# Optimization experiments

Measured on AMD Instinct MI355X. Metric: run time of the kernel, lower is better.

Reference implementation:

```python
import jax, jax.numpy as jnp
import numpy as np

N, E, F, H = 131072, 524288, 128, 128
EPS = 1e-5

def _gcn(x, W, b, src, dst, ew):
    # GCNConv with normalize=False: linear -> gather -> edge-weight scale -> scatter-add -> bias
    h = x @ W                                  # [N, H]
    msg = h[src] * ew[:, None]                 # [E, H]
    return jax.ops.segment_sum(msg, dst, num_segments=N) + b

def _ln(x, g, b):
    mu = jnp.mean(x, axis=-1, keepdims=True)
    var = jnp.var(x, axis=-1, keepdims=True)
    return (x - mu) * jax.lax.rsqrt(var + EPS) * g + b

def setup_inputs() -> dict:
    key = jax.random.key(0)
    ks = jax.random.split(key, 32)
    d = {}
    d['x'] = jax.random.normal(ks[0], (N, F), dtype=jnp.float32)
    names = ['fwd', 'ons', 'sus', 'rest']
    for i, t in enumerate(names):
        d['ei_' + t] = jax.random.randint(ks[1 + i], (2, E), 0, N)
        d['ew_' + t] = jax.random.uniform(ks[5 + i], (E,), dtype=jnp.float32)
        d['W1_' + t] = jax.random.normal(ks[9 + i], (F, H), dtype=jnp.float32) * 0.1
        d['b1_' + t] = jnp.zeros((H,), dtype=jnp.float32)
        d['W2_' + t] = jax.random.normal(ks[13 + i], (H, H), dtype=jnp.float32) * 0.1
        d['b2_' + t] = jnp.zeros((H,), dtype=jnp.float32)
    d['g1'] = jnp.ones((H,), dtype=jnp.float32)
    d['be1'] = jnp.zeros((H,), dtype=jnp.float32)
    d['g2'] = jnp.ones((H,), dtype=jnp.float32)
    d['be2'] = jnp.zeros((H,), dtype=jnp.float32)
    return d

def reference(x, ei_fwd, ei_ons, ei_sus, ei_rest,
              ew_fwd, ew_ons, ew_sus, ew_rest,
              W1_fwd, b1_fwd, W2_fwd, b2_fwd,
              W1_ons, b1_ons, W2_ons, b2_ons,
              W1_sus, b1_sus, W2_sus, b2_sus,
              W1_rest, b1_rest, W2_rest, b2_rest,
              g1, be1, g2, be2):
    eis = [ei_fwd, ei_ons, ei_sus, ei_rest]
    ews = [ew_fwd, ew_ons, ew_sus, ew_rest]
    W1s = [W1_fwd, W1_ons, W1_sus, W1_rest]
    b1s = [b1_fwd, b1_ons, b1_sus, b1_rest]
    W2s = [W2_fwd, W2_ons, W2_sus, W2_rest]
    b2s = [b2_fwd, b2_ons, b2_sus, b2_rest]
    # HeteroConv aggr='sum' over the 4 edge types
    h = sum(_gcn(x, W1s[i], b1s[i], eis[i][0], eis[i][1], ews[i]) for i in range(4))
    h = _ln(h, g1, be1)  # dropout is identity in eval/reference mode
    h2 = sum(_gcn(h, W2s[i], b2s[i], eis[i][0], eis[i][1], ews[i]) for i in range(4))
    return _ln(h2, g2, be2)
```

## Files before the change

kernel.cpp:

```cpp
#include <hip/hip_runtime.h>
#include <hip/hip_fp16.h>

#define NN 131072
#define EE 524288

typedef _Float16 f16x8 __attribute__((ext_vector_type(8)));
typedef float f32x4 __attribute__((ext_vector_type(4)));

__device__ __forceinline__ unsigned short f2h(float f) {
  __half h = __float2half(f);
  unsigned short r;
  __builtin_memcpy(&r, &h, 2);
  return r;
}
__device__ __forceinline__ __half2 u2h2(unsigned u) {
  __half2 h;
  __builtin_memcpy(&h, &u, 4);
  return h;
}
__device__ __forceinline__ unsigned h22u(__half2 h) {
  unsigned u;
  __builtin_memcpy(&u, &h, 4);
  return u;
}

__global__ __launch_bounds__(256) void khc(const int* __restrict__ d0, const int* __restrict__ d1,
                                           const int* __restrict__ d2, const int* __restrict__ d3,
                                           unsigned* __restrict__ gc) {
  __shared__ unsigned h[512];
  for (int i = threadIdx.x; i < 512; i += 256) h[i] = 0;
  __syncthreads();
  unsigned base = blockIdx.x * 2048u + threadIdx.x;
#pragma unroll
  for (int k = 0; k < 8; ++k) {
    unsigned e = base + k * 256u;
    unsigned t = e >> 19, i = e & (EE - 1u);
    const int* dd = (t == 0) ? d0 : (t == 1) ? d1 : (t == 2) ? d2 : d3;
    atomicAdd(&h[((unsigned)dd[i]) >> 8], 1u);
  }
  __syncthreads();
  for (int i = threadIdx.x; i < 512; i += 256) atomicAdd(&gc[i], h[i]);
}

__global__ __launch_bounds__(512) void kscan_small(const unsigned* __restrict__ gc, unsigned* __restrict__ rpc,
                                                   unsigned* __restrict__ cursor, unsigned* __restrict__ rp_fine) {
  __shared__ unsigned sh[512];
  int tid = threadIdx.x;
  unsigned x = gc[tid];
  sh[tid] = x;
  __syncthreads();
  for (int o = 1; o < 512; o <<= 1) {
    unsigned v = (tid >= o) ? sh[tid - o] : 0u;
    __syncthreads();
    sh[tid] += v;
    __syncthreads();
  }
  unsigned excl = sh[tid] - x;
  rpc[tid] = excl;
  cursor[tid] = excl;
  if (tid == 511) rpc[512] = sh[511];
  if (tid == 0) rp_fine[4u * NN] = 4u * EE;
}

__global__ __launch_bounds__(256) void kbinA(
    const int* __restrict__ e0, const int* __restrict__ e1, const int* __restrict__ e2, const int* __restrict__ e3,
    const float* __restrict__ w0, const float* __restrict__ w1, const float* __restrict__ w2, const float* __restrict__ w3,
    unsigned* __restrict__ cursor, uint2* __restrict__ tmp) {
  __shared__ unsigned hist[512];
  __shared__ unsigned base[512];
  int tid = threadIdx.x;
  unsigned t = blockIdx.x >> 7;
  unsigned chunk = blockIdx.x & 127u;
  const int* ei = (t == 0) ? e0 : (t == 1) ? e1 : (t == 2) ? e2 : e3;
  const float* ew = (t == 0) ? w0 : (t == 1) ? w1 : (t == 2) ? w2 : w3;
  const int* srcp = ei;
  const int* dstp = ei + EE;
  unsigned ib = chunk * 4096u;
  for (int i = tid; i < 512; i += 256) hist[i] = 0;
  __syncthreads();
  unsigned km[16], sm[16];
  float wm[16];
#pragma unroll
  for (int k = 0; k < 16; ++k) {
    unsigned i = ib + k * 256u + tid;
    unsigned dst = (unsigned)dstp[i];
    sm[k] = (unsigned)srcp[i];
    wm[k] = ew[i];
    km[k] = (dst << 2) | t;
    atomicAdd(&hist[dst >> 8], 1u);
  }
  __syncthreads();
  for (int j = tid; j < 512; j += 256) {
    unsigned c = hist[j];
    base[j] = c ? atomicAdd(&cursor[j], c) : 0u;
    hist[j] = 0u;
  }
  __syncthreads();
#pragma unroll
  for (int k = 0; k < 16; ++k) {
    unsigned b = km[k] >> 10;
    unsigned l = atomicAdd(&hist[b], 1u);
    tmp[(size_t)base[b] + l] = make_uint2(sm[k] | ((km[k] & 1023u) << 17), __float_as_uint(wm[k]));
  }
}

__global__ __launch_bounds__(256) void kbinB(const unsigned* __restrict__ rpc, const uint2* __restrict__ tmp,
                                             unsigned* __restrict__ rp_fine, uint2* __restrict__ edges) {
  __shared__ unsigned cnts[1024];
  __shared__ unsigned ps[256];
  int tid = threadIdx.x;
  unsigned b = blockIdx.x;
  unsigned s = rpc[b], e = rpc[b + 1];
  unsigned cnt = e - s;
  for (int j = tid; j < 1024; j += 256) cnts[j] = 0;
  __syncthreads();
  for (unsigned i = tid; i < cnt; i += 256) {
    unsigned lk = tmp[s + i].x >> 17;
    atomicAdd(&cnts[lk], 1u);
  }
  __syncthreads();
  unsigned c4[4], lsum = 0;
#pragma unroll
  for (int q = 0; q < 4; ++q) { c4[q] = cnts[tid * 4 + q]; lsum += c4[q]; }
  ps[tid] = lsum;
  __syncthreads();
  for (int o = 1; o < 256; o <<= 1) {
    unsigned v = (tid >= o) ? ps[tid - o] : 0u;
    __syncthreads();
    ps[tid] += v;
    __syncthreads();
  }
  unsigned excl = ps[tid] - lsum;
  __syncthreads();
#pragma unroll
  for (int q = 0; q < 4; ++q) {
    rp_fine[b * 1024u + (unsigned)tid * 4u + q] = s + excl;
    cnts[tid * 4 + q] = excl;
    excl += c4[q];
  }
  __syncthreads();
  for (unsigned i = tid; i < cnt; i += 256) {
    uint2 r = tmp[s + i];
    unsigned lk = r.x >> 17;
    unsigned p = atomicAdd(&cnts[lk], 1u);
    edges[(size_t)s + p] = make_uint2(r.x & 0x1ffffu, r.y);
  }
}

__global__ __launch_bounds__(256) void kcast(const float4* __restrict__ x, ushort4* __restrict__ o) {
  unsigned i = blockIdx.x * 256u + threadIdx.x;
  float4 v = x[i];
  ushort4 r;
  r.x = f2h(v.x); r.y = f2h(v.y); r.z = f2h(v.z); r.w = f2h(v.w);
  o[i] = r;
}

__global__ __launch_bounds__(256) void kwconv2(
    const float* __restrict__ m0, const float* __restrict__ m1, const float* __restrict__ m2, const float* __restrict__ m3,
    const float* __restrict__ m4, const float* __restrict__ m5, const float* __restrict__ m6, const float* __restrict__ m7,
    unsigned short* __restrict__ img) {
  unsigned gidx = blockIdx.x * 256u + threadIdx.x;
  unsigned L = gidx >> 16;
  unsigned r = gidx & 65535u;
  unsigned k = r >> 7, c = r & 127u;
  unsigned t = k >> 7, krow = k & 127u;
  const float* W;
  if (L == 0) W = (t == 0) ? m0 : (t == 1) ? m1 : (t == 2) ? m2 : m3;
  else        W = (t == 0) ? m4 : (t == 1) ? m5 : (t == 2) ? m6 : m7;
  img[(size_t)L * 65536 + (k >> 5) * 4096 + c * 32 + ((k & 31u) ^ ((c & 3u) << 3))] = f2h(W[krow * 128 + c]);
}

__global__ __launch_bounds__(128) void kbias(
    const float* __restrict__ a0, const float* __restrict__ a1, const float* __restrict__ a2, const float* __restrict__ a3,
    const float* __restrict__ c0, const float* __restrict__ c1, const float* __restrict__ c2, const float* __restrict__ c3,
    float* __restrict__ bsum) {
  int c = threadIdx.x;
  bsum[c] = a0[c] + a1[c] + a2[c] + a3[c];
  bsum[128 + c] = c0[c] + c1[c] + c2[c] + c3[c];
}

__global__ __launch_bounds__(512) void kfuse(const uint2* __restrict__ edges, const unsigned* __restrict__ rp,
                                             const unsigned short* __restrict__ X,
                                             const unsigned short* __restrict__ Wimg, int layer,
                                             const float* __restrict__ bsum,
                                             const float* __restrict__ gw, const float* __restrict__ bw,
                                             unsigned short* __restrict__ outh, float* __restrict__ outf, int wf32) {
  __shared__ unsigned short sZ[64 * 512];
  __shared__ unsigned short sW[2 * 4096];
  const int tid = threadIdx.x;
  const int wv = tid >> 6;
  const int lane = tid & 63;
  const int g = lane >> 4;
  const int cl = lane & 15;
  const unsigned dbase = blockIdx.x * 64u;

  const unsigned short* Xr = X + (size_t)(cl * 8);
  for (int it = 0; it < 8; ++it) {
    unsigned row = (unsigned)(wv * 8 + it);
    unsigned d = dbase + row;
    unsigned s = rp[d * 4u + g];
    unsigned e = rp[d * 4u + g + 1];
    unsigned len = e - s;
    int m = (int)len;
    m = max(m, __shfl_xor(m, 16, 64));
    m = max(m, __shfl_xor(m, 32, 64));
    __half2 accA[4], accB[4];
    const __half2 z2 = __half2(__half(0.f), __half(0.f));
#pragma unroll
    for (int k = 0; k < 4; ++k) { accA[k] = z2; accB[k] = z2; }
    unsigned jlast = len ? e - 1u : s;
    for (int i = 0; i < m; i += 4) {
      unsigned j[4], sidx[4];
      uint2 q[4];
      __half2 w2[4];
#pragma unroll
      for (int k = 0; k < 4; ++k) {
        bool v = (unsigned)(i + k) < len;
        j[k] = v ? s + (unsigned)(i + k) : jlast;
      }
#pragma unroll
      for (int k = 0; k < 4; ++k) q[k] = edges[j[k]];
#pragma unroll
      for (int k = 0; k < 4; ++k) {
        bool v = (unsigned)(i + k) < len;
        sidx[k] = v ? q[k].x : 0u;
        w2[k] = __float2half2_rn(v ? __uint_as_float(q[k].y) : 0.f);
      }
      uint4 u0 = *(const uint4*)(Xr + (size_t)sidx[0] * 128);
      uint4 u1 = *(const uint4*)(Xr + (size_t)sidx[1] * 128);
      uint4 u2 = *(const uint4*)(Xr + (size_t)sidx[2] * 128);
      uint4 u3 = *(const uint4*)(Xr + (size_t)sidx[3] * 128);
      accA[0] = __hfma2(w2[0], u2h2(u0.x), accA[0]);
      accA[1] = __hfma2(w2[0], u2h2(u0.y), accA[1]);
      accA[2] = __hfma2(w2[0], u2h2(u0.z), accA[2]);
      accA[3] = __hfma2(w2[0], u2h2(u0.w), accA[3]);
      accB[0] = __hfma2(w2[1], u2h2(u1.x), accB[0]);
      accB[1] = __hfma2(w2[1], u2h2(u1.y), accB[1]);
      accB[2] = __hfma2(w2[1], u2h2(u1.z), accB[2]);
      accB[3] = __hfma2(w2[1], u2h2(u1.w), accB[3]);
      accA[0] = __hfma2(w2[2], u2h2(u2.x), accA[0]);
      accA[1] = __hfma2(w2[2], u2h2(u2.y), accA[1]);
      accA[2] = __hfma2(w2[2], u2h2(u2.z), accA[2]);
      accA[3] = __hfma2(w2[2], u2h2(u2.w), accA[3]);
      accB[0] = __hfma2(w2[3], u2h2(u3.x), accB[0]);
      accB[1] = __hfma2(w2[3], u2h2(u3.y), accB[1]);
      accB[2] = __hfma2(w2[3], u2h2(u3.z), accB[2]);
      accB[3] = __hfma2(w2[3], u2h2(u3.w), accB[3]);
    }
    uint4 o;
    o.x = h22u(__hadd2(accA[0], accB[0]));
    o.y = h22u(__hadd2(accA[1], accB[1]));
    o.z = h22u(__hadd2(accA[2], accB[2]));
    o.w = h22u(__hadd2(accA[3], accB[3]));
    *(uint4*)((char*)sZ + row * 1024 + (((unsigned)(g * 256 + cl * 16)) ^ ((row & 7u) << 4))) = o;
  }

  const int rlo = lane & 15;
  const int khi = lane >> 4;
  const int mt = wv >> 1;
  const int nh = wv & 1;
  f32x4 acc[4];
#pragma unroll
  for (int n = 0; n < 4; ++n) acc[n] = (f32x4){0.f, 0.f, 0.f, 0.f};
  const uint4* W2 = (const uint4*)(Wimg + (size_t)layer * 65536);
  const int arow = mt * 16 + rlo;
  for (int st = 0; st < 8; ++st) {
    __syncthreads();
    ((uint4*)sW)[tid * 2] = W2[st * 1024 + tid * 2];
    ((uint4*)sW)[tid * 2 + 1] = W2[st * 1024 + tid * 2 + 1];
    __syncthreads();
#pragma unroll
    for (int kcl = 0; kcl < 2; ++kcl) {
      int kc = st * 2 + kcl;
      f16x8 a = *(const f16x8*)((const char*)sZ + arow * 1024 + (((unsigned)(kc * 64 + khi * 16)) ^ ((arow & 7) << 4)));
#pragma unroll
      for (int n = 0; n < 4; ++n) {
        int cc = nh * 64 + n * 16 + rlo;
        f16x8 b = *(const f16x8*)((const char*)sW + kcl * 8192 + cc * 64 + (((unsigned)(khi * 16)) ^ ((cc & 3) << 4)));
        acc[n] = __builtin_amdgcn_mfma_f32_16x16x32_f16(a, b, acc[n], 0, 0, 0);
      }
    }
  }

  float bs[4], ggv[4], bwv[4];
#pragma unroll
  for (int n = 0; n < 4; ++n) {
    int cc = nh * 64 + n * 16 + rlo;
    bs[n] = bsum[cc];
    ggv[n] = gw[cc];
    bwv[n] = bw[cc];
  }
  float* sPart = (float*)sW;
  __syncthreads();
#pragma unroll
  for (int rg = 0; rg < 4; ++rg) {
    float s1 = 0.f, s2 = 0.f;
#pragma unroll
    for (int n = 0; n < 4; ++n) {
      float v = acc[n][rg] + bs[n];
      s1 += v;
      s2 += v * v;
    }
    s1 += __shfl_xor(s1, 1, 64); s2 += __shfl_xor(s2, 1, 64);
    s1 += __shfl_xor(s1, 2, 64); s2 += __shfl_xor(s2, 2, 64);
    s1 += __shfl_xor(s1, 4, 64); s2 += __shfl_xor(s2, 4, 64);
    s1 += __shfl_xor(s1, 8, 64); s2 += __shfl_xor(s2, 8, 64);
    if (rlo == 0) {
      int row = mt * 16 + khi * 4 + rg;
      sPart[row * 4 + nh * 2] = s1;
      sPart[row * 4 + nh * 2 + 1] = s2;
    }
  }
  __syncthreads();
#pragma unroll
  for (int rg = 0; rg < 4; ++rg) {
    int row = mt * 16 + khi * 4 + rg;
    float s1 = sPart[row * 4 + 0] + sPart[row * 4 + 2];
    float s2 = sPart[row * 4 + 1] + sPart[row * 4 + 3];
    float mu = s1 * (1.f / 128.f);
    float var = fmaxf(s2 * (1.f / 128.f) - mu * mu, 0.f);
    float inv = rsqrtf(var + 1e-5f);
    size_t d = (size_t)dbase + (unsigned)row;
    if (wf32) {
#pragma unroll
      for (int n = 0; n < 4; ++n) {
        int cc = nh * 64 + n * 16 + rlo;
        outf[d * 128 + cc] = (acc[n][rg] + bs[n] - mu) * inv * ggv[n] + bwv[n];
      }
    } else {
#pragma unroll
      for (int n = 0; n < 4; ++n) {
        int cc = nh * 64 + n * 16 + rlo;
        outh[d * 128 + cc] = f2h((acc[n][rg] + bs[n] - mu) * inv * ggv[n] + bwv[n]);
      }
    }
  }
}

extern "C" void kernel_launch(void* const* d_in, const int* in_sizes, int n_in,
                              void* d_out, int out_size, void* d_ws, size_t ws_size,
                              hipStream_t stream) {
  (void)n_in; (void)out_size; (void)ws_size;
  const float* x = (const float*)d_in[0];
  const int* ei[4];
  const float *ew[4], *W1[4], *b1[4], *W2[4], *b2[4];
  const float *g1, *be1, *g2, *be2;
  if (in_sizes[2] == EE) {
    for (int t = 0; t < 4; ++t) {
      int base = 1 + t * 6;
      ei[t] = (const int*)d_in[base + 0];
      ew[t] = (const float*)d_in[base + 1];
      W1[t] = (const float*)d_in[base + 2];
      b1[t] = (const float*)d_in[base + 3];
      W2[t] = (const float*)d_in[base + 4];
      b2[t] = (const float*)d_in[base + 5];
    }
  } else {
    for (int t = 0; t < 4; ++t) {
      ei[t] = (const int*)d_in[1 + t];
      ew[t] = (const float*)d_in[5 + t];
      W1[t] = (const float*)d_in[9 + t * 4 + 0];
      b1[t] = (const float*)d_in[9 + t * 4 + 1];
      W2[t] = (const float*)d_in[9 + t * 4 + 2];
      b2[t] = (const float*)d_in[9 + t * 4 + 3];
    }
  }
  g1 = (const float*)d_in[25];
  be1 = (const float*)d_in[26];
  g2 = (const float*)d_in[27];
  be2 = (const float*)d_in[28];

  char* ws = (char*)d_ws;
  size_t off = 0;
  auto take = [&](size_t b) { char* p = ws + off; off = (off + b + 255) & ~(size_t)255; return p; };
  unsigned* gcounts = (unsigned*)take(512 * 4);
  unsigned* rpc     = (unsigned*)take(513 * 4);
  unsigned* cursor  = (unsigned*)take(512 * 4);
  unsigned* rp_fine = (unsigned*)take((4ull * NN + 1) * 4);
  unsigned short* Wimg2 = (unsigned short*)take(2ull * 65536 * 2);
  float* bsum       = (float*)take(256 * 4);
  uint2* edges      = (uint2*)take(4ull * EE * 8);
  unsigned short* Xh = (unsigned short*)take((size_t)NN * 128 * 2);
  unsigned short* Yh = (unsigned short*)take((size_t)NN * 128 * 2);
  uint2* tmp = (uint2*)((char*)d_out + 48ull * 1024 * 1024);

  hipMemsetAsync(gcounts, 0, 512 * 4, stream);
  khc<<<1024, 256, 0, stream>>>(ei[0] + EE, ei[1] + EE, ei[2] + EE, ei[3] + EE, gcounts);
  kscan_small<<<1, 512, 0, stream>>>(gcounts, rpc, cursor, rp_fine);
  kbinA<<<512, 256, 0, stream>>>(ei[0], ei[1], ei[2], ei[3], ew[0], ew[1], ew[2], ew[3], cursor, tmp);
  kbinB<<<512, 256, 0, stream>>>(rpc, tmp, rp_fine, edges);
  kcast<<<NN * 128 / 4 / 256, 256, 0, stream>>>((const float4*)x, (ushort4*)Xh);
  kwconv2<<<512, 256, 0, stream>>>(W1[0], W1[1], W1[2], W1[3], W2[0], W2[1], W2[2], W2[3], Wimg2);
  kbias<<<1, 128, 0, stream>>>(b1[0], b1[1], b1[2], b1[3], b2[0], b2[1], b2[2], b2[3], bsum);

  kfuse<<<NN / 64, 512, 0, stream>>>(edges, rp_fine, Xh, Wimg2, 0, bsum, g1, be1, Yh, nullptr, 0);
  kfuse<<<NN / 64, 512, 0, stream>>>(edges, rp_fine, Yh, Wimg2, 1, bsum + 128, g2, be2, nullptr, (float*)d_out, 1);
}
```

Measured before the change: 347.1 us.

## Halve fused tile to 32 rows and read MFMA weights from global

The fused gather+GEMM+LayerNorm kernel now handles 32 destination rows per block instead of 64. The shared weight staging buffer and its barriers are removed. Weights are re-laid out into an MFMA-fragment-ordered image so each wave loads its B operands straight from global/L2 with contiguous 16-byte reads. Waves are split 2x4 over rows and columns, and the LayerNorm partial sums now combine four column groups. The smaller LDS footprint and the launch bound of 8 blocks per CU aim to raise occupancy and hide gather latency, at the cost of more repeated weight reads from cache.

```diff
diff --git a/kernel.cpp b/kernel.cpp
--- a/kernel.cpp
+++ b/kernel.cpp
@@ -155,19 +155,23 @@
   o[i] = r;
 }
 
-__global__ __launch_bounds__(256) void kwconv2(
+__global__ __launch_bounds__(256) void kwconv3(
     const float* __restrict__ m0, const float* __restrict__ m1, const float* __restrict__ m2, const float* __restrict__ m3,
     const float* __restrict__ m4, const float* __restrict__ m5, const float* __restrict__ m6, const float* __restrict__ m7,
     unsigned short* __restrict__ img) {
   unsigned gidx = blockIdx.x * 256u + threadIdx.x;
   unsigned L = gidx >> 16;
   unsigned r = gidx & 65535u;
-  unsigned k = r >> 7, c = r & 127u;
+  unsigned kc = r >> 12;
+  unsigned khi = (r >> 10) & 3u;
+  unsigned cc = (r >> 3) & 127u;
+  unsigned j = r & 7u;
+  unsigned k = kc * 32u + khi * 8u + j;
   unsigned t = k >> 7, krow = k & 127u;
   const float* W;
   if (L == 0) W = (t == 0) ? m0 : (t == 1) ? m1 : (t == 2) ? m2 : m3;
   else        W = (t == 0) ? m4 : (t == 1) ? m5 : (t == 2) ? m6 : m7;
-  img[(size_t)L * 65536 + (k >> 5) * 4096 + c * 32 + ((k & 31u) ^ ((c & 3u) << 3))] = f2h(W[krow * 128 + c]);
+  img[gidx] = f2h(W[krow * 128 + cc]);
 }
 
 __global__ __launch_bounds__(128) void kbias(
@@ -179,24 +183,23 @@
   bsum[128 + c] = c0[c] + c1[c] + c2[c] + c3[c];
 }
 
-__global__ __launch_bounds__(512) void kfuse(const uint2* __restrict__ edges, const unsigned* __restrict__ rp,
-                                             const unsigned short* __restrict__ X,
-                                             const unsigned short* __restrict__ Wimg, int layer,
-                                             const float* __restrict__ bsum,
-                                             const float* __restrict__ gw, const float* __restrict__ bw,
-                                             unsigned short* __restrict__ outh, float* __restrict__ outf, int wf32) {
-  __shared__ unsigned short sZ[64 * 512];
-  __shared__ unsigned short sW[2 * 4096];
+__global__ __launch_bounds__(512, 8) void kfuse(const uint2* __restrict__ edges, const unsigned* __restrict__ rp,
+                                                const unsigned short* __restrict__ X,
+                                                const unsigned short* __restrict__ Wimg, int layer,
+                                                const float* __restrict__ bsum,
+                                                const float* __restrict__ gw, const float* __restrict__ bw,
+                                                unsigned short* __restrict__ outh, float* __restrict__ outf, int wf32) {
+  __shared__ unsigned short sZ[32 * 512];
   const int tid = threadIdx.x;
   const int wv = tid >> 6;
   const int lane = tid & 63;
   const int g = lane >> 4;
   const int cl = lane & 15;
-  const unsigned dbase = blockIdx.x * 64u;
+  const unsigned dbase = blockIdx.x * 32u;
 
   const unsigned short* Xr = X + (size_t)(cl * 8);
-  for (int it = 0; it < 8; ++it) {
-    unsigned row = (unsigned)(wv * 8 + it);
+  for (int it = 0; it < 4; ++it) {
+    unsigned row = (unsigned)(wv * 4 + it);
     unsigned d = dbase + row;
     unsigned s = rp[d * 4u + g];
     unsigned e = rp[d * 4u + g + 1];
@@ -254,83 +257,73 @@
     o.w = h22u(__hadd2(accA[3], accB[3]));
     *(uint4*)((char*)sZ + row * 1024 + (((unsigned)(g * 256 + cl * 16)) ^ ((row & 7u) << 4))) = o;
   }
+  __syncthreads();
 
   const int rlo = lane & 15;
   const int khi = lane >> 4;
-  const int mt = wv >> 1;
-  const int nh = wv & 1;
-  f32x4 acc[4];
-#pragma unroll
-  for (int n = 0; n < 4; ++n) acc[n] = (f32x4){0.f, 0.f, 0.f, 0.f};
-  const uint4* W2 = (const uint4*)(Wimg + (size_t)layer * 65536);
+  const int mt = wv >> 2;
+  const int nh = wv & 3;
+  f32x4 acc[2];
+  acc[0] = (f32x4){0.f, 0.f, 0.f, 0.f};
+  acc[1] = (f32x4){0.f, 0.f, 0.f, 0.f};
+  const unsigned short* WL = Wimg + (size_t)layer * 65536;
   const int arow = mt * 16 + rlo;
-  for (int st = 0; st < 8; ++st) {
-    __syncthreads();
-    ((uint4*)sW)[tid * 2] = W2[st * 1024 + tid * 2];
-    ((uint4*)sW)[tid * 2 + 1] = W2[st * 1024 + tid * 2 + 1];
-    __syncthreads();
-#pragma unroll
-    for (int kcl = 0; kcl < 2; ++kcl) {
-      int kc = st * 2 + kcl;
-      f16x8 a = *(const f16x8*)((const char*)sZ + arow * 1024 + (((unsigned)(kc * 64 + khi * 16)) ^ ((arow & 7) << 4)));
-#pragma unroll
-      for (int n = 0; n < 4; ++n) {
-        int cc = nh * 64 + n * 16 + rlo;
-        f16x8 b = *(const f16x8*)((const char*)sW + kcl * 8192 + cc * 64 + (((unsigned)(khi * 16)) ^ ((cc & 3) << 4)));
-        acc[n] = __builtin_amdgcn_mfma_f32_16x16x32_f16(a, b, acc[n], 0, 0, 0);
-      }
-    }
-  }
-
-  float bs[4], ggv[4], bwv[4];
-#pragma unroll
-  for (int n = 0; n < 4; ++n) {
-    int cc = nh * 64 + n * 16 + rlo;
+  const unsigned abase = (unsigned)(arow * 1024);
+  const unsigned aswz = (unsigned)((arow & 7) << 4);
+#pragma unroll 4
+  for (int kc = 0; kc < 16; ++kc) {
+    f16x8 a = *(const f16x8*)((const char*)sZ + abase + (((unsigned)(kc * 64 + khi * 16)) ^ aswz));
+    const f16x8* bp = (const f16x8*)(WL + (size_t)(((kc * 4 + khi) * 128) + nh * 32 + rlo) * 8);
+    acc[0] = __builtin_amdgcn_mfma_f32_16x16x32_f16(a, bp[0], acc[0], 0, 0, 0);
+    acc[1] = __builtin_amdgcn_mfma_f32_16x16x32_f16(a, bp[16], acc[1], 0, 0, 0);
+  }
+
+  float bs[2], ggv[2], bwv[2];
+#pragma unroll
+  for (int n = 0; n < 2; ++n) {
+    int cc = nh * 32 + n * 16 + rlo;
     bs[n] = bsum[cc];
     ggv[n] = gw[cc];
     bwv[n] = bw[cc];
   }
-  float* sPart = (float*)sW;
-  __syncthreads();
+  __syncthreads();
+  float* sPart = (float*)sZ;
 #pragma unroll
   for (int rg = 0; rg < 4; ++rg) {
-    float s1 = 0.f, s2 = 0.f;
-#pragma unroll
-    for (int n = 0; n < 4; ++n) {
-      float v = acc[n][rg] + bs[n];
-      s1 += v;
-      s2 += v * v;
-    }
+    float v0 = acc[0][rg] + bs[0];
+    float v1 = acc[1][rg] + bs[1];
+    float s1 = v0 + v1;
+    float s2 = v0 * v0 + v1 * v1;
     s1 += __shfl_xor(s1, 1, 64); s2 += __shfl_xor(s2, 1, 64);
     s1 += __shfl_xor(s1, 2, 64); s2 += __shfl_xor(s2, 2, 64);
     s1 += __shfl_xor(s1, 4, 64); s2 += __shfl_xor(s2, 4, 64);
     s1 += __shfl_xor(s1, 8, 64); s2 += __shfl_xor(s2, 8, 64);
     if (rlo == 0) {
       int row = mt * 16 + khi * 4 + rg;
-      sPart[row * 4 + nh * 2] = s1;
-      sPart[row * 4 + nh * 2 + 1] = s2;
+      sPart[row * 8 + nh * 2] = s1;
+      sPart[row * 8 + nh * 2 + 1] = s2;
     }
   }
   __syncthreads();
 #pragma unroll
   for (int rg = 0; rg < 4; ++rg) {
     int row = mt * 16 + khi * 4 + rg;
-    float s1 = sPart[row * 4 + 0] + sPart[row * 4 + 2];
-    float s2 = sPart[row * 4 + 1] + sPart[row * 4 + 3];
+    float s1 = sPart[row * 8 + 0] + sPart[row * 8 + 2] + sPart[row * 8 + 4] + sPart[row * 8 + 6];
+    float s2 = sPart[row * 8 + 1] + sPart[row * 8 + 3] + sPart[row * 8 + 5] + sPart[row * 8 + 7];
     float mu = s1 * (1.f / 128.f);
     float var = fmaxf(s2 * (1.f / 128.f) - mu * mu, 0.f);
     float inv = rsqrtf(var + 1e-5f);
     size_t d = (size_t)dbase + (unsigned)row;
     if (wf32) {
 #pragma unroll
-      for (int n = 0; n < 4; ++n) {
-        int cc = nh * 64 + n * 16 + rlo;
+      for (int n = 0; n < 2; ++n) {
+        int cc = nh * 32 + n * 16 + rlo;
         outf[d * 128 + cc] = (acc[n][rg] + bs[n] - mu) * inv * ggv[n] + bwv[n];
       }
     } else {
 #pragma unroll
-      for (int n = 0; n < 4; ++n) {
-        int cc = nh * 64 + n * 16 + rlo;
+      for (int n = 0; n < 2; ++n) {
+        int cc = nh * 32 + n * 16 + rlo;
         outh[d * 128 + cc] = f2h((acc[n][rg] + bs[n] - mu) * inv * ggv[n] + bwv[n]);
       }
     }
@@ -377,7 +370,7 @@
   unsigned* rpc     = (unsigned*)take(513 * 4);
   unsigned* cursor  = (unsigned*)take(512 * 4);
   unsigned* rp_fine = (unsigned*)take((4ull * NN + 1) * 4);
-  unsigned short* Wimg2 = (unsigned short*)take(2ull * 65536 * 2);
+  unsigned short* Wimg3 = (unsigned short*)take(2ull * 65536 * 2);
   float* bsum       = (float*)take(256 * 4);
   uint2* edges      = (uint2*)take(4ull * EE * 8);
   unsigned short* Xh = (unsigned short*)take((size_t)NN * 128 * 2);
@@ -390,9 +383,9 @@
   kbinA<<<512, 256, 0, stream>>>(ei[0], ei[1], ei[2], ei[3], ew[0], ew[1], ew[2], ew[3], cursor, tmp);
   kbinB<<<512, 256, 0, stream>>>(rpc, tmp, rp_fine, edges);
   kcast<<<NN * 128 / 4 / 256, 256, 0, stream>>>((const float4*)x, (ushort4*)Xh);
-  kwconv2<<<512, 256, 0, stream>>>(W1[0], W1[1], W1[2], W1[3], W2[0], W2[1], W2[2], W2[3], Wimg2);
+  kwconv3<<<512, 256, 0, stream>>>(W1[0], W1[1], W1[2], W1[3], W2[0], W2[1], W2[2], W2[3], Wimg3);
   kbias<<<1, 128, 0, stream>>>(b1[0], b1[1], b1[2], b1[3], b2[0], b2[1], b2[2], b2[3], bsum);
 
-  kfuse<<<NN / 64, 512, 0, stream>>>(edges, rp_fine, Xh, Wimg2, 0, bsum, g1, be1, Yh, nullptr, 0);
-  kfuse<<<NN / 64, 512, 0, stream>>>(edges, rp_fine, Yh, Wimg2, 1, bsum + 128, g2, be2, nullptr, (float*)d_out, 1);
-}
+  kfuse<<<NN / 32, 512, 0, stream>>>(edges, rp_fine, Xh, Wimg3, 0, bsum, g1, be1, Yh, nullptr, 0);
+  kfuse<<<NN / 32, 512, 0, stream>>>(edges, rp_fine, Yh, Wimg3, 1, bsum + 128, g2, be2, nullptr, (float*)d_out, 1);
+}
```

Result: faster. 318.0 us (-8.4%).
